# Performance work log

Hardware: AMD Instinct MI355X
Metric: run time of the kernel (lower is better)

The kernel has to match this reference:

```python
import jax, jax.numpy as jnp
import numpy as np

N = 20000          # nodes
E = 320000         # edges
H = 128            # hidden_channels
A = 512            # aerial feature dim
SPOT = 20000
DIST_UNIT = 50
NEMB = SPOT // DIST_UNIT
RATIO = 0.25       # neighbor_ratio


def setup_inputs() -> dict:
    key = jax.random.key(0)
    ks = jax.random.split(key, 12)
    x = jax.random.normal(ks[0], (N, H), jnp.float32)
    edge_index = jax.random.randint(ks[1], (2, E), 0, N)
    distances = jax.random.randint(ks[2], (E,), 0, SPOT)
    aerial_emb = jax.random.normal(ks[3], (N, A), jnp.float32)
    s = lambda k, shape, fan: jax.random.normal(k, shape, jnp.float32) / np.sqrt(fan).astype(np.float32)
    W_lin = s(ks[4], (H, H), H)
    b_lin = jnp.zeros((H,), jnp.float32)
    W_q = s(ks[5], (H + A + H, H), H + A + H)
    b_q = jnp.zeros((H,), jnp.float32)
    W_v = s(ks[6], (H, H), H)
    b_v = jnp.zeros((H,), jnp.float32)
    dist_table = jax.random.normal(ks[7], (NEMB, H), jnp.float32)  # init.normal_ like torch
    W_l = s(ks[8], (H, H), H)   # SAGE lin_l (neighbor aggr), with bias
    b_l = jnp.zeros((H,), jnp.float32)
    W_r = s(ks[9], (H, H), H)   # SAGE lin_r (root), no bias in PyG default
    return dict(x=x, edge_index=edge_index, distances=distances, aerial_emb=aerial_emb,
                W_lin=W_lin, b_lin=b_lin, W_q=W_q, b_q=b_q, W_v=W_v, b_v=b_v,
                dist_table=dist_table, W_l=W_l, b_l=b_l, W_r=W_r)


def reference(x, edge_index, distances, aerial_emb, W_lin, b_lin, W_q, b_q, W_v, b_v, dist_table, W_l, b_l, W_r):
    n = x.shape[0]
    e = edge_index.shape[1]
    k = int(e * RATIO)  # static: number of sampled edges

    x = x @ W_lin + b_lin                                  # [N, H]
    src, tgt = edge_index[0], edge_index[1]
    source_x = x[src]                                      # [E, H]
    target_x = x[tgt]                                      # [E, H]
    source_aerial = aerial_emb[src]                        # [E, A]
    dist_x = dist_table[distances // DIST_UNIT]            # [E, H]

    query = jnp.concatenate([source_x, source_aerial, dist_x], axis=1) @ W_q + b_q  # [E, H]
    value = target_x @ W_v + b_v                           # [E, H]
    logits = -jnp.linalg.norm(query - value, axis=1)       # [E]
    logprob = jax.nn.log_softmax(logits, axis=0)

    # torch.multinomial(prob, k) without replacement == Gumbel top-k on log-probs
    u = jax.random.uniform(jax.random.key(42), (e,), jnp.float32)
    gumbel = -jnp.log(-jnp.log(u + 1e-20) + 1e-20)
    _, sel = jax.lax.top_k(logprob + gumbel, k)            # [k] selected edge ids
    src_s = src[sel]
    tgt_s = tgt[sel]

    # SAGEConv (mean aggregation): out = lin_l(mean_j x_j) + lin_r(x)
    msg = jax.ops.segment_sum(x[src_s], tgt_s, num_segments=n)              # [N, H]
    deg = jax.ops.segment_sum(jnp.ones((k,), x.dtype), tgt_s, num_segments=n)
    aggr = msg / jnp.maximum(deg, 1.0)[:, None]
    out = aggr @ W_l + b_l + x @ W_r                       # [N, H]
    return out
```

## Files before the change

kernel.cpp:

```cpp
#include <hip/hip_runtime.h>
#include <stdint.h>

#define N_NODES 20000
#define E_EDGES 320000
#define H_DIM 128
#define A_DIM 512
#define NEMB_N 400
#define K_SEL 80000u
#define NB1 16384
#define NB2 16384
#define CAND_MAX 8192
#define LO_F (-128.0f)
#define SCALE1 (16384.0f / 160.0f)
#define KN_M 32

struct SelState {
    int b1; unsigned cum1; unsigned r1;
    int b2; unsigned cum2; unsigned r2;
    unsigned long long T;
};

__device__ __forceinline__ uint32_t rotl32(uint32_t x, int r) {
    return (x << r) | (x >> (32 - r));
}

__device__ __forceinline__ void threefry2x32(uint32_t k0, uint32_t k1,
                                             uint32_t& x0, uint32_t& x1) {
    uint32_t ks0 = k0, ks1 = k1, ks2 = k0 ^ k1 ^ 0x1BD11BDAu;
    x0 += ks0; x1 += ks1;
    x0 += x1; x1 = rotl32(x1, 13); x1 ^= x0;
    x0 += x1; x1 = rotl32(x1, 15); x1 ^= x0;
    x0 += x1; x1 = rotl32(x1, 26); x1 ^= x0;
    x0 += x1; x1 = rotl32(x1, 6);  x1 ^= x0;
    x0 += ks1; x1 += ks2 + 1u;
    x0 += x1; x1 = rotl32(x1, 17); x1 ^= x0;
    x0 += x1; x1 = rotl32(x1, 29); x1 ^= x0;
    x0 += x1; x1 = rotl32(x1, 16); x1 ^= x0;
    x0 += x1; x1 = rotl32(x1, 24); x1 ^= x0;
    x0 += ks2; x1 += ks0 + 2u;
    x0 += x1; x1 = rotl32(x1, 13); x1 ^= x0;
    x0 += x1; x1 = rotl32(x1, 15); x1 ^= x0;
    x0 += x1; x1 = rotl32(x1, 26); x1 ^= x0;
    x0 += x1; x1 = rotl32(x1, 6);  x1 ^= x0;
    x0 += ks0; x1 += ks1 + 3u;
    x0 += x1; x1 = rotl32(x1, 17); x1 ^= x0;
    x0 += x1; x1 = rotl32(x1, 29); x1 ^= x0;
    x0 += x1; x1 = rotl32(x1, 16); x1 ^= x0;
    x0 += x1; x1 = rotl32(x1, 24); x1 ^= x0;
    x0 += ks1; x1 += ks2 + 4u;
    x0 += x1; x1 = rotl32(x1, 13); x1 ^= x0;
    x0 += x1; x1 = rotl32(x1, 15); x1 ^= x0;
    x0 += x1; x1 = rotl32(x1, 26); x1 ^= x0;
    x0 += x1; x1 = rotl32(x1, 6);  x1 ^= x0;
    x0 += ks2; x1 += ks0 + 5u;
}

__global__ __launch_bounds__(128) void k_node(
    const float* __restrict__ x, const float* __restrict__ aerial,
    const float* __restrict__ Wlin, const float* __restrict__ blin,
    const float* __restrict__ Wq, const float* __restrict__ bq,
    const float* __restrict__ Wv, const float* __restrict__ bv,
    float* __restrict__ xl32, float* __restrict__ q32, float* __restrict__ v32) {
    __shared__ float bufA[H_DIM][KN_M + 4];
    __shared__ float bufX[H_DIM][KN_M + 4];
    const int tid = threadIdx.x;
    const int mg = tid >> 5;
    const int jj = tid & 31;
    const int nb = mg * 8;
    const int n0 = blockIdx.x * KN_M;
    const int c0 = jj, c1 = jj + 32, c2 = jj + 64, c3 = jj + 96;

    for (int m = 0; m < KN_M; ++m)
        bufA[tid][m] = x[(size_t)(n0 + m) * H_DIM + tid];
    __syncthreads();

    float accL[4][8];
    {
        float b0 = blin[c0], b1 = blin[c1], b2 = blin[c2], b3 = blin[c3];
#pragma unroll
        for (int i = 0; i < 8; ++i) {
            accL[0][i] = b0; accL[1][i] = b1; accL[2][i] = b2; accL[3][i] = b3;
        }
    }
#pragma unroll 4
    for (int k = 0; k < H_DIM; ++k) {
        const float4 xa = *(const float4*)&bufA[k][nb];
        const float4 xb = *(const float4*)&bufA[k][nb + 4];
        const float w0 = Wlin[k * H_DIM + c0];
        const float w1 = Wlin[k * H_DIM + c1];
        const float w2 = Wlin[k * H_DIM + c2];
        const float w3 = Wlin[k * H_DIM + c3];
        const float xv[8] = {xa.x, xa.y, xa.z, xa.w, xb.x, xb.y, xb.z, xb.w};
#pragma unroll
        for (int i = 0; i < 8; ++i) {
            accL[0][i] = fmaf(xv[i], w0, accL[0][i]);
            accL[1][i] = fmaf(xv[i], w1, accL[1][i]);
            accL[2][i] = fmaf(xv[i], w2, accL[2][i]);
            accL[3][i] = fmaf(xv[i], w3, accL[3][i]);
        }
    }
#pragma unroll
    for (int c = 0; c < 4; ++c) {
        const int col = jj + c * 32;
#pragma unroll
        for (int i = 0; i < 8; ++i) {
            xl32[(size_t)(n0 + nb + i) * H_DIM + col] = accL[c][i];
            bufX[col][nb + i] = accL[c][i];
        }
    }
    __syncthreads();

    float accV[4][8], accQ[4][8];
    {
        float v0 = bv[c0], v1 = bv[c1], v2 = bv[c2], v3 = bv[c3];
        float q0 = bq[c0], q1 = bq[c1], q2 = bq[c2], q3 = bq[c3];
#pragma unroll
        for (int i = 0; i < 8; ++i) {
            accV[0][i] = v0; accV[1][i] = v1; accV[2][i] = v2; accV[3][i] = v3;
            accQ[0][i] = q0; accQ[1][i] = q1; accQ[2][i] = q2; accQ[3][i] = q3;
        }
    }
#pragma unroll 2
    for (int k = 0; k < H_DIM; ++k) {
        const float4 xa = *(const float4*)&bufX[k][nb];
        const float4 xb = *(const float4*)&bufX[k][nb + 4];
        const float wv0 = Wv[k * H_DIM + c0];
        const float wv1 = Wv[k * H_DIM + c1];
        const float wv2 = Wv[k * H_DIM + c2];
        const float wv3 = Wv[k * H_DIM + c3];
        const float wq0 = Wq[k * H_DIM + c0];
        const float wq1 = Wq[k * H_DIM + c1];
        const float wq2 = Wq[k * H_DIM + c2];
        const float wq3 = Wq[k * H_DIM + c3];
        const float xv[8] = {xa.x, xa.y, xa.z, xa.w, xb.x, xb.y, xb.z, xb.w};
#pragma unroll
        for (int i = 0; i < 8; ++i) {
            accV[0][i] = fmaf(xv[i], wv0, accV[0][i]);
            accV[1][i] = fmaf(xv[i], wv1, accV[1][i]);
            accV[2][i] = fmaf(xv[i], wv2, accV[2][i]);
            accV[3][i] = fmaf(xv[i], wv3, accV[3][i]);
            accQ[0][i] = fmaf(xv[i], wq0, accQ[0][i]);
            accQ[1][i] = fmaf(xv[i], wq1, accQ[1][i]);
            accQ[2][i] = fmaf(xv[i], wq2, accQ[2][i]);
            accQ[3][i] = fmaf(xv[i], wq3, accQ[3][i]);
        }
    }
#pragma unroll
    for (int c = 0; c < 4; ++c) {
        const int col = jj + c * 32;
#pragma unroll
        for (int i = 0; i < 8; ++i)
            v32[(size_t)(n0 + nb + i) * H_DIM + col] = accV[c][i];
    }

    for (int ch = 0; ch < 4; ++ch) {
        __syncthreads();
        for (int m = 0; m < KN_M; ++m)
            bufA[tid][m] = aerial[(size_t)(n0 + m) * A_DIM + ch * H_DIM + tid];
        __syncthreads();
        const float* Wqc = Wq + (size_t)(H_DIM + ch * H_DIM) * H_DIM;
#pragma unroll 4
        for (int k = 0; k < H_DIM; ++k) {
            const float4 xa = *(const float4*)&bufA[k][nb];
            const float4 xb = *(const float4*)&bufA[k][nb + 4];
            const float w0 = Wqc[k * H_DIM + c0];
            const float w1 = Wqc[k * H_DIM + c1];
            const float w2 = Wqc[k * H_DIM + c2];
            const float w3 = Wqc[k * H_DIM + c3];
            const float xv[8] = {xa.x, xa.y, xa.z, xa.w, xb.x, xb.y, xb.z, xb.w};
#pragma unroll
            for (int i = 0; i < 8; ++i) {
                accQ[0][i] = fmaf(xv[i], w0, accQ[0][i]);
                accQ[1][i] = fmaf(xv[i], w1, accQ[1][i]);
                accQ[2][i] = fmaf(xv[i], w2, accQ[2][i]);
                accQ[3][i] = fmaf(xv[i], w3, accQ[3][i]);
            }
        }
    }
#pragma unroll
    for (int c = 0; c < 4; ++c) {
        const int col = jj + c * 32;
#pragma unroll
        for (int i = 0; i < 8; ++i)
            q32[(size_t)(n0 + nb + i) * H_DIM + col] = accQ[c][i];
    }
}

__global__ __launch_bounds__(128) void k_dist(
    const float* __restrict__ dtab, const float* __restrict__ Wq,
    float* __restrict__ dq32) {
    __shared__ float dsT[H_DIM][8];
    const int j = threadIdx.x;
    const int n0 = blockIdx.x * 8;
#pragma unroll
    for (int m = 0; m < 8; ++m) dsT[j][m] = dtab[(size_t)(n0 + m) * H_DIM + j];
    __syncthreads();
    float acc[8];
#pragma unroll
    for (int m = 0; m < 8; ++m) acc[m] = 0.0f;
    for (int k = 0; k < H_DIM; ++k) {
        float w = Wq[(size_t)(H_DIM + A_DIM + k) * H_DIM + j];
        const float4* xp = (const float4*)&dsT[k][0];
        float4 a0 = xp[0], a1 = xp[1];
        acc[0] = fmaf(a0.x, w, acc[0]); acc[1] = fmaf(a0.y, w, acc[1]);
        acc[2] = fmaf(a0.z, w, acc[2]); acc[3] = fmaf(a0.w, w, acc[3]);
        acc[4] = fmaf(a1.x, w, acc[4]); acc[5] = fmaf(a1.y, w, acc[5]);
        acc[6] = fmaf(a1.z, w, acc[6]); acc[7] = fmaf(a1.w, w, acc[7]);
    }
#pragma unroll
    for (int m = 0; m < 8; ++m) dq32[(size_t)(n0 + m) * H_DIM + j] = acc[m];
}

__device__ __forceinline__ int bin1_of(float s) {
    float t = (s - LO_F) * SCALE1;
    int b = (int)t;
    return min(max(b, 0), NB1 - 1);
}
__device__ __forceinline__ int bin2_of(float s, int b1) {
    float t = (s - LO_F) * SCALE1;
    float frac = t - (float)b1;
    int b = (int)(frac * (float)NB2);
    return min(max(b, 0), NB2 - 1);
}

__global__ __launch_bounds__(256) void k_score(
    const int* __restrict__ ei, const int* __restrict__ dist,
    const float* __restrict__ q32, const float* __restrict__ v32,
    const float* __restrict__ dq32,
    unsigned long long* __restrict__ keys, float* __restrict__ s32o,
    unsigned* __restrict__ hist1) {
    const int half = threadIdx.x >> 5, lane = threadIdx.x & 31;
    const int e = blockIdx.x * 8 + half;
    const int s = ei[e], t = ei[E_EDGES + e];
    const int db = dist[e] / 50;
    const float4* qp = (const float4*)(q32 + (size_t)s * H_DIM);
    const float4* vp = (const float4*)(v32 + (size_t)t * H_DIM);
    const float4* dp = (const float4*)(dq32 + (size_t)db * H_DIM);
    float4 q = qp[lane], v = vp[lane], d = dp[lane];
    float dx = q.x + d.x - v.x;
    float dy = q.y + d.y - v.y;
    float dz = q.z + d.z - v.z;
    float dw = q.w + d.w - v.w;
    float ss = fmaf(dx, dx, fmaf(dy, dy, fmaf(dz, dz, dw * dw)));
#pragma unroll
    for (int o = 16; o > 0; o >>= 1) ss += __shfl_xor(ss, o, 64);
    uint32_t r0 = 0u, r1 = (uint32_t)e;
    threefry2x32(0u, 42u, r0, r1);
    uint32_t fb = ((r0 ^ r1) >> 9) | 0x3f800000u;
    float uu = __uint_as_float(fb) - 1.0f;
    if (lane == 0) {
        float nrm = sqrtf(ss);
        float a = -logf(uu + 1e-20f);
        float g = -logf(a + 1e-20f);
        float score = g - nrm;
        int ib = __float_as_int(score);
        unsigned m32 = (ib < 0) ? ~(unsigned)ib : ((unsigned)ib | 0x80000000u);
        keys[e] = ((unsigned long long)m32 << 32) | (unsigned)(0xFFFFFFFFu - (unsigned)e);
        s32o[e] = score;
        atomicAdd(&hist1[bin1_of(score)], 1u);
    }
}

__global__ __launch_bounds__(256) void k_hist2(const float* __restrict__ s32,
                                               const SelState* __restrict__ st,
                                               unsigned* __restrict__ hist2) {
    int e = blockIdx.x * 256 + threadIdx.x;
    if (e >= E_EDGES) return;
    float s = s32[e];
    int b1 = bin1_of(s);
    if (b1 != st->b1) return;
    atomicAdd(&hist2[bin2_of(s, b1)], 1u);
}

__global__ __launch_bounds__(256) void k_scan(const unsigned* __restrict__ hist,
                                              SelState* st, int phase) {
    __shared__ unsigned csum[256];
    __shared__ unsigned bins[64];
    __shared__ int selc;
    __shared__ unsigned cumbase;
    const int t = threadIdx.x;
    const unsigned target = (phase == 1) ? K_SEL : st->r1;
    unsigned s = 0;
    for (int i = 0; i < 64; ++i) s += hist[t * 64 + i];
    csum[t] = s;
    __syncthreads();
    if (t == 0) {
        unsigned cum = 0; int c = 255;
        for (; c >= 0; --c) {
            if (cum + csum[c] >= target) break;
            cum += csum[c];
        }
        selc = c; cumbase = cum;
    }
    __syncthreads();
    if (t < 64) bins[t] = hist[selc * 64 + t];
    __syncthreads();
    if (t == 0) {
        unsigned cum = cumbase; int b = -1;
        for (int i = 63; i >= 0; --i) {
            if (cum + bins[i] >= target) { b = selc * 64 + i; break; }
            cum += bins[i];
        }
        unsigned r = target - cum;
        if (phase == 1) { st->b1 = b; st->cum1 = cum; st->r1 = r; }
        else           { st->b2 = b; st->cum2 = cum; st->r2 = r; }
    }
}

__global__ __launch_bounds__(256) void k_collect(
    const float* __restrict__ s32, const unsigned long long* __restrict__ keys,
    const SelState* __restrict__ st, unsigned long long* __restrict__ cand,
    unsigned* __restrict__ cnt) {
    int e = blockIdx.x * 256 + threadIdx.x;
    if (e >= E_EDGES) return;
    float s = s32[e];
    int b1 = bin1_of(s);
    if (b1 != st->b1) return;
    if (bin2_of(s, b1) != st->b2) return;
    unsigned p = atomicAdd(cnt, 1u);
    if (p < CAND_MAX) cand[p] = keys[e];
}

__global__ __launch_bounds__(256) void k_thresh(
    const unsigned long long* __restrict__ cand, const unsigned* __restrict__ cnt,
    SelState* st) {
    int c = (int)min(*cnt, (unsigned)CAND_MAX);
    unsigned r2 = st->r2;
    for (int i = threadIdx.x; i < c; i += blockDim.x) {
        unsigned long long ki = cand[i];
        unsigned g = 0;
        for (int j = 0; j < c; ++j) g += (cand[j] > ki);
        if (g == r2 - 1) st->T = ki;
    }
}

__global__ __launch_bounds__(256) void k_scatter(
    const int* __restrict__ ei, const unsigned long long* __restrict__ keys,
    const SelState* __restrict__ st, const float* __restrict__ xl32,
    float* __restrict__ msg, float* __restrict__ deg) {
    const int wid = threadIdx.x >> 6, lane = threadIdx.x & 63;
    const int e = blockIdx.x * 4 + wid;
    if (keys[e] >= st->T) {
        int sidx = ei[e], tidx = ei[E_EDGES + e];
        const float* xp = xl32 + (size_t)sidx * H_DIM;
        float* mp = msg + (size_t)tidx * H_DIM;
        const int h = lane * 2;
        atomicAdd(&mp[h], xp[h]);
        atomicAdd(&mp[h + 1], xp[h + 1]);
        if (lane == 0) atomicAdd(&deg[tidx], 1.0f);
    }
}

__global__ __launch_bounds__(128) void k_out(
    const float* __restrict__ msg, const float* __restrict__ deg,
    const float* __restrict__ xl32, const float* __restrict__ Wl,
    const float* __restrict__ bl, const float* __restrict__ Wr,
    float* __restrict__ out) {
    __shared__ float axT[H_DIM][8];
    __shared__ float xxT[H_DIM][8];
    const int j = threadIdx.x;
    const int n0 = blockIdx.x * 8;
#pragma unroll
    for (int m = 0; m < 8; ++m) {
        float d = fmaxf(deg[n0 + m], 1.0f);
        axT[j][m] = msg[(size_t)(n0 + m) * H_DIM + j] / d;
        xxT[j][m] = xl32[(size_t)(n0 + m) * H_DIM + j];
    }
    __syncthreads();
    float acc[8];
    float bj = bl[j];
#pragma unroll
    for (int m = 0; m < 8; ++m) acc[m] = bj;
    for (int k = 0; k < H_DIM; ++k) {
        float wl = Wl[k * H_DIM + j];
        float wr = Wr[k * H_DIM + j];
        const float4* ap = (const float4*)&axT[k][0];
        const float4* xp = (const float4*)&xxT[k][0];
        float4 a0 = ap[0], a1 = ap[1];
        float4 x0 = xp[0], x1 = xp[1];
        acc[0] = fmaf(a0.x, wl, fmaf(x0.x, wr, acc[0]));
        acc[1] = fmaf(a0.y, wl, fmaf(x0.y, wr, acc[1]));
        acc[2] = fmaf(a0.z, wl, fmaf(x0.z, wr, acc[2]));
        acc[3] = fmaf(a0.w, wl, fmaf(x0.w, wr, acc[3]));
        acc[4] = fmaf(a1.x, wl, fmaf(x1.x, wr, acc[4]));
        acc[5] = fmaf(a1.y, wl, fmaf(x1.y, wr, acc[5]));
        acc[6] = fmaf(a1.z, wl, fmaf(x1.z, wr, acc[6]));
        acc[7] = fmaf(a1.w, wl, fmaf(x1.w, wr, acc[7]));
    }
#pragma unroll
    for (int m = 0; m < 8; ++m) out[(size_t)(n0 + m) * H_DIM + j] = acc[m];
}

extern "C" void kernel_launch(void* const* d_in, const int* in_sizes, int n_in,
                              void* d_out, int out_size, void* d_ws, size_t ws_size,
                              hipStream_t stream) {
    const float* x      = (const float*)d_in[0];
    const int*   ei     = (const int*)d_in[1];
    const int*   dist   = (const int*)d_in[2];
    const float* aerial = (const float*)d_in[3];
    const float* Wlin   = (const float*)d_in[4];
    const float* blin   = (const float*)d_in[5];
    const float* Wq     = (const float*)d_in[6];
    const float* bq     = (const float*)d_in[7];
    const float* Wv     = (const float*)d_in[8];
    const float* bv     = (const float*)d_in[9];
    const float* dtab   = (const float*)d_in[10];
    const float* Wl     = (const float*)d_in[11];
    const float* bl     = (const float*)d_in[12];
    const float* Wr     = (const float*)d_in[13];
    float* out = (float*)d_out;

    char* ws = (char*)d_ws;
    size_t off = 0;
    auto alloc = [&](size_t bytes) -> void* {
        void* p = ws + off;
        off += (bytes + 255) & ~(size_t)255;
        return p;
    };
    float* q32  = (float*)alloc((size_t)N_NODES * H_DIM * 4);
    float* v32  = (float*)alloc((size_t)N_NODES * H_DIM * 4);
    float* dq32 = (float*)alloc((size_t)NEMB_N * H_DIM * 4);
    unsigned long long* keys = (unsigned long long*)alloc((size_t)E_EDGES * 8);
    float* xl32 = (float*)alloc((size_t)N_NODES * H_DIM * 4);
    float* s32  = (float*)alloc((size_t)E_EDGES * 4);
    char* zbase = ws + off;
    float* msg  = (float*)alloc((size_t)N_NODES * H_DIM * 4);
    float* deg  = (float*)alloc((size_t)N_NODES * 4);
    unsigned* hist1 = (unsigned*)alloc((size_t)NB1 * 4);
    unsigned* hist2 = (unsigned*)alloc((size_t)NB2 * 4);
    unsigned long long* cand = (unsigned long long*)alloc((size_t)CAND_MAX * 8);
    unsigned* counters = (unsigned*)alloc(256);
    SelState* st = (SelState*)alloc(256);
    size_t zlen = (size_t)((ws + off) - zbase);

    hipMemsetAsync(zbase, 0, zlen, stream);

    k_node<<<N_NODES / KN_M, 128, 0, stream>>>(x, aerial, Wlin, blin, Wq, bq, Wv, bv,
                                               xl32, q32, v32);
    k_dist<<<NEMB_N / 8, 128, 0, stream>>>(dtab, Wq, dq32);
    k_score<<<E_EDGES / 8, 256, 0, stream>>>(ei, dist, q32, v32, dq32, keys, s32, hist1);
    k_scan<<<1, 256, 0, stream>>>(hist1, st, 1);
    k_hist2<<<(E_EDGES + 255) / 256, 256, 0, stream>>>(s32, st, hist2);
    k_scan<<<1, 256, 0, stream>>>(hist2, st, 2);
    k_collect<<<(E_EDGES + 255) / 256, 256, 0, stream>>>(s32, keys, st, cand, &counters[0]);
    k_thresh<<<1, 256, 0, stream>>>(cand, &counters[0], st);
    k_scatter<<<E_EDGES / 4, 256, 0, stream>>>(ei, keys, st, xl32, msg, deg);
    k_out<<<N_NODES / 8, 128, 0, stream>>>(msg, deg, xl32, Wl, bl, Wr, out);
}
```

Measured before the change: 570.7 us.

## Batch four edges per 32-lane group in score kernel and split histogram pass

Each 32-lane group in the score kernel now handles four edges instead of one. All gathers for those edges are issued up front so more loads are in flight, and the threefry RNG and log work is spread across four lanes instead of being redundant per group. The histogram atomics move out of the score kernel into a separate k_hist1 pass over the stored scores. This trades one extra launch and an extra read of the score array for better memory-level parallelism and less divergent serial work in the gather kernel.

Measured after the change: 499.3 us. 12.5% less time.

```diff
diff --git a/kernel.cpp b/kernel.cpp
--- a/kernel.cpp
+++ b/kernel.cpp
@@ -227,38 +227,66 @@
     const int* __restrict__ ei, const int* __restrict__ dist,
     const float* __restrict__ q32, const float* __restrict__ v32,
     const float* __restrict__ dq32,
-    unsigned long long* __restrict__ keys, float* __restrict__ s32o,
-    unsigned* __restrict__ hist1) {
+    unsigned long long* __restrict__ keys, float* __restrict__ s32o) {
     const int half = threadIdx.x >> 5, lane = threadIdx.x & 31;
-    const int e = blockIdx.x * 8 + half;
-    const int s = ei[e], t = ei[E_EDGES + e];
-    const int db = dist[e] / 50;
-    const float4* qp = (const float4*)(q32 + (size_t)s * H_DIM);
-    const float4* vp = (const float4*)(v32 + (size_t)t * H_DIM);
-    const float4* dp = (const float4*)(dq32 + (size_t)db * H_DIM);
-    float4 q = qp[lane], v = vp[lane], d = dp[lane];
-    float dx = q.x + d.x - v.x;
-    float dy = q.y + d.y - v.y;
-    float dz = q.z + d.z - v.z;
-    float dw = q.w + d.w - v.w;
-    float ss = fmaf(dx, dx, fmaf(dy, dy, fmaf(dz, dz, dw * dw)));
-#pragma unroll
-    for (int o = 16; o > 0; o >>= 1) ss += __shfl_xor(ss, o, 64);
-    uint32_t r0 = 0u, r1 = (uint32_t)e;
+    const int e0 = blockIdx.x * 32 + half * 4;
+    int sidx[4], tidx[4], db[4];
+#pragma unroll
+    for (int i = 0; i < 4; ++i) {
+        sidx[i] = ei[e0 + i];
+        tidx[i] = ei[E_EDGES + e0 + i];
+        db[i] = dist[e0 + i] / 50;
+    }
+    float4 q[4], v[4], d[4];
+#pragma unroll
+    for (int i = 0; i < 4; ++i)
+        q[i] = ((const float4*)(q32 + (size_t)sidx[i] * H_DIM))[lane];
+#pragma unroll
+    for (int i = 0; i < 4; ++i)
+        v[i] = ((const float4*)(v32 + (size_t)tidx[i] * H_DIM))[lane];
+#pragma unroll
+    for (int i = 0; i < 4; ++i)
+        d[i] = ((const float4*)(dq32 + (size_t)db[i] * H_DIM))[lane];
+    uint32_t r0 = 0u, r1 = (uint32_t)(e0 + (lane & 3));
     threefry2x32(0u, 42u, r0, r1);
     uint32_t fb = ((r0 ^ r1) >> 9) | 0x3f800000u;
-    float uu = __uint_as_float(fb) - 1.0f;
-    if (lane == 0) {
-        float nrm = sqrtf(ss);
-        float a = -logf(uu + 1e-20f);
+    float uu_l = __uint_as_float(fb) - 1.0f;
+
+    float ss[4];
+#pragma unroll
+    for (int i = 0; i < 4; ++i) {
+        float dx = q[i].x + d[i].x - v[i].x;
+        float dy = q[i].y + d[i].y - v[i].y;
+        float dz = q[i].z + d[i].z - v[i].z;
+        float dw = q[i].w + d[i].w - v[i].w;
+        float t = fmaf(dx, dx, fmaf(dy, dy, fmaf(dz, dz, dw * dw)));
+#pragma unroll
+        for (int o = 16; o > 0; o >>= 1) t += __shfl_xor(t, o, 64);
+        ss[i] = t;
+    }
+    if (lane < 4) {
+        float myss = ss[0];
+        if (lane == 1) myss = ss[1];
+        if (lane == 2) myss = ss[2];
+        if (lane == 3) myss = ss[3];
+        float nrm = sqrtf(myss);
+        float a = -logf(uu_l + 1e-20f);
         float g = -logf(a + 1e-20f);
         float score = g - nrm;
         int ib = __float_as_int(score);
         unsigned m32 = (ib < 0) ? ~(unsigned)ib : ((unsigned)ib | 0x80000000u);
-        keys[e] = ((unsigned long long)m32 << 32) | (unsigned)(0xFFFFFFFFu - (unsigned)e);
+        const int e = e0 + lane;
+        keys[e] = ((unsigned long long)m32 << 32) |
+                  (unsigned)(0xFFFFFFFFu - (unsigned)e);
         s32o[e] = score;
-        atomicAdd(&hist1[bin1_of(score)], 1u);
-    }
+    }
+}
+
+__global__ __launch_bounds__(256) void k_hist1(const float* __restrict__ s32,
+                                               unsigned* __restrict__ hist1) {
+    int e = blockIdx.x * 256 + threadIdx.x;
+    if (e >= E_EDGES) return;
+    atomicAdd(&hist1[bin1_of(s32[e])], 1u);
 }
 
 __global__ __launch_bounds__(256) void k_hist2(const float* __restrict__ s32,
@@ -438,7 +466,8 @@
     k_node<<<N_NODES / KN_M, 128, 0, stream>>>(x, aerial, Wlin, blin, Wq, bq, Wv, bv,
                                                xl32, q32, v32);
     k_dist<<<NEMB_N / 8, 128, 0, stream>>>(dtab, Wq, dq32);
-    k_score<<<E_EDGES / 8, 256, 0, stream>>>(ei, dist, q32, v32, dq32, keys, s32, hist1);
+    k_score<<<E_EDGES / 32, 256, 0, stream>>>(ei, dist, q32, v32, dq32, keys, s32);
+    k_hist1<<<(E_EDGES + 255) / 256, 256, 0, stream>>>(s32, hist1);
     k_scan<<<1, 256, 0, stream>>>(hist1, st, 1);
     k_hist2<<<(E_EDGES + 255) / 256, 256, 0, stream>>>(s32, st, hist2);
     k_scan<<<1, 256, 0, stream>>>(hist2, st, 2);
```
